# Kernel tuning notes

Hardware: AMD Instinct MI355X
Metric: run time of the kernel (lower is better)

## Reference

```python
import jax, jax.numpy as jnp
import numpy as np

D_MODEL = 1024
H = 16
D_K = D_MODEL // H
B, S = 4, 2048
NEG = -1000000000.0


def setup_inputs() -> dict:
    key = jax.random.key(0)
    ks = jax.random.split(key, 12)
    scale = 1.0 / np.sqrt(D_MODEL)
    inp = {
        "query": jax.random.normal(ks[0], (B, S, D_MODEL), jnp.float32),
        "key": jax.random.normal(ks[1], (B, S, D_MODEL), jnp.float32),
        "value": jax.random.normal(ks[2], (B, S, D_MODEL), jnp.float32),
        # causal lower-triangular mask, shape (B, S, S); forward unsqueezes head dim
        "mask": jnp.broadcast_to(jnp.tril(jnp.ones((S, S), jnp.int32)), (B, S, S)),
        "Wq": jax.random.normal(ks[3], (D_MODEL, D_MODEL), jnp.float32) * scale,
        "bq": jnp.zeros((D_MODEL,), jnp.float32),
        "Wk": jax.random.normal(ks[4], (D_MODEL, D_MODEL), jnp.float32) * scale,
        "bk": jnp.zeros((D_MODEL,), jnp.float32),
        "Wv": jax.random.normal(ks[5], (D_MODEL, D_MODEL), jnp.float32) * scale,
        "bv": jnp.zeros((D_MODEL,), jnp.float32),
        "Wo": jax.random.normal(ks[6], (D_MODEL, D_MODEL), jnp.float32) * scale,
        "bo": jnp.zeros((D_MODEL,), jnp.float32),
    }
    return inp


def reference(query, key, value, mask, Wq, bq, Wk, bk, Wv, bv, Wo, bo):
    b, s, _ = query.shape
    # projections (torch Linear: x @ W.T + b); split into heads -> (b, h, s, d_k)
    def proj(x, W, bias):
        return (x @ W.T + bias).reshape(b, -1, H, D_K).transpose(0, 2, 1, 3)

    Q = proj(query, Wq, bq)
    K = proj(key, Wk, bk)
    V = proj(value, Wv, bv)

    scores = jnp.einsum("bhqd,bhkd->bhqk", Q, K) / np.sqrt(D_K)
    m = mask[:, None, :, :]  # (b, 1, s, s)
    scores = jnp.where(m == 0, NEG, scores)
    attn = jax.nn.softmax(scores, axis=-1)
    x = jnp.einsum("bhqk,bhkd->bhqd", attn, V)
    x = x.transpose(0, 2, 1, 3).reshape(b, -1, D_MODEL)
    return x @ Wo.T + bo
```

## Files before the change

### kernel.cpp

```cpp
#include <hip/hip_runtime.h>
#include <hip/hip_bf16.h>

#define DMODEL 1024
#define NH 16
#define DKH 64
#define NB 4
#define SEQ 2048
#define MTOT (NB*SEQ)

typedef __bf16 bf16_t;
typedef __bf16 bf16x8 __attribute__((ext_vector_type(8)));
typedef float f32x4 __attribute__((ext_vector_type(4)));

__device__ __forceinline__ void async_copy16(void* lds, const void* g) {
    __builtin_amdgcn_global_load_lds(
        (const __attribute__((address_space(1))) unsigned int*)g,
        (__attribute__((address_space(3))) unsigned int*)lds, 16, 0, 0);
}

__device__ __forceinline__ float fast_exp2(float x) {
    return __builtin_amdgcn_exp2f(x);
}

__device__ __forceinline__ float rsum16(float v) {
    v += __shfl_xor(v, 1);
    v += __shfl_xor(v, 2);
    v += __shfl_xor(v, 4);
    v += __shfl_xor(v, 8);
    return v;
}

__global__ void cvt_kernel(const float* __restrict__ s0, const float* __restrict__ s1,
                           const float* __restrict__ s2, const float* __restrict__ s3,
                           bf16_t* __restrict__ d0, bf16_t* __restrict__ d1,
                           bf16_t* __restrict__ d2, bf16_t* __restrict__ d3, int n)
{
    const float* s = (blockIdx.y == 0) ? s0 : (blockIdx.y == 1) ? s1 :
                     (blockIdx.y == 2) ? s2 : s3;
    bf16_t* d = (blockIdx.y == 0) ? d0 : (blockIdx.y == 1) ? d1 :
                (blockIdx.y == 2) ? d2 : d3;
    int i = (blockIdx.x * 256 + threadIdx.x) * 8;
    if (i < n) {
        float4 a = *(const float4*)&s[i];
        float4 b = *(const float4*)&s[i + 4];
        union { bf16_t h[8]; uint4 u; } t;
        t.h[0]=(bf16_t)a.x; t.h[1]=(bf16_t)a.y; t.h[2]=(bf16_t)a.z; t.h[3]=(bf16_t)a.w;
        t.h[4]=(bf16_t)b.x; t.h[5]=(bf16_t)b.y; t.h[6]=(bf16_t)b.z; t.h[7]=(bf16_t)b.w;
        *(uint4*)&d[i] = t.u;
    }
}

template<int OUT_MODE>
__global__ __launch_bounds__(256, 2)
void gemm_bt(const bf16_t* __restrict__ A, const bf16_t* __restrict__ W,
             const float* __restrict__ bias, void* __restrict__ out,
             int M, int N, int K, float scale)
{
    __shared__ bf16_t As[2][128 * 64];
    __shared__ bf16_t Ws[2][128 * 64];

    const int tid  = threadIdx.x;
    const int wave = tid >> 6;
    const int lane = tid & 63;
    const int ln   = lane & 15;
    const int quad = lane >> 4;
    const int wm   = (wave >> 1) * 64;
    const int wn   = (wave & 1) * 64;
    const int bm   = blockIdx.x * 128;
    const int bn   = blockIdx.y * 128;
    const int srow = wave * 8 + (lane >> 3);
    const int sg   = (lane & 7) * 8;

    f32x4 acc[4][4] = {};

    #pragma unroll
    for (int rr = 0; rr < 4; ++rr) {
        int row = rr * 32 + srow;
        async_copy16(&As[0][(size_t)(rr * 32 + wave * 8) * 64],
                     &A[(size_t)(bm + row) * K + sg]);
        async_copy16(&Ws[0][(size_t)(rr * 32 + wave * 8) * 64],
                     &W[(size_t)(bn + row) * K + sg]);
    }

    int cur = 0;
    for (int k0 = 0; k0 < K; k0 += 64, cur ^= 1) {
        __syncthreads();

        if (k0 + 64 < K) {
            #pragma unroll
            for (int rr = 0; rr < 4; ++rr) {
                int row = rr * 32 + srow;
                async_copy16(&As[cur ^ 1][(size_t)(rr * 32 + wave * 8) * 64],
                             &A[(size_t)(bm + row) * K + k0 + 64 + sg]);
                async_copy16(&Ws[cur ^ 1][(size_t)(rr * 32 + wave * 8) * 64],
                             &W[(size_t)(bn + row) * K + k0 + 64 + sg]);
            }
        }

        bf16x8 af[2][4], wf[2][4];
        #pragma unroll
        for (int h = 0; h < 2; ++h)
            #pragma unroll
            for (int u = 0; u < 4; ++u) {
                af[h][u] = *(const bf16x8*)&As[cur][(wm + u * 16 + ln) * 64 + h * 32 + quad * 8];
                wf[h][u] = *(const bf16x8*)&Ws[cur][(wn + u * 16 + ln) * 64 + h * 32 + quad * 8];
            }
        #pragma unroll
        for (int h = 0; h < 2; ++h)
            #pragma unroll
            for (int im = 0; im < 4; ++im)
                #pragma unroll
                for (int jn = 0; jn < 4; ++jn)
                    acc[im][jn] = __builtin_amdgcn_mfma_f32_16x16x32_bf16(
                        af[h][im], wf[h][jn], acc[im][jn], 0, 0, 0);
    }

    #pragma unroll
    for (int jn = 0; jn < 4; ++jn) {
        int n = bn + wn + jn * 16 + ln;
        float bv = bias[n];
        #pragma unroll
        for (int im = 0; im < 4; ++im) {
            #pragma unroll
            for (int r = 0; r < 4; ++r) {
                int m = bm + wm + im * 16 + quad * 4 + r;
                float v = (acc[im][jn][r] + bv) * scale;
                if (OUT_MODE == 0) {
                    int b = m >> 11, s = m & (SEQ - 1);
                    int h = n >> 6, d = n & 63;
                    ((bf16_t*)out)[(((size_t)(b * NH + h)) * SEQ + s) * DKH + d] = (bf16_t)v;
                } else if (OUT_MODE == 2) {
                    int b = m >> 11, s = m & (SEQ - 1);
                    int h = n >> 6, d = n & 63;
                    ((bf16_t*)out)[(((size_t)(b * NH + h)) * DKH + d) * SEQ + s] = (bf16_t)v;
                } else {
                    ((float*)out)[(size_t)m * N + n] = v;
                }
            }
        }
    }
}

__global__ __launch_bounds__(256, 3)
void attn_kernel(const bf16_t* __restrict__ Q, const bf16_t* __restrict__ Km,
                 const bf16_t* __restrict__ Vt, bf16_t* __restrict__ X)
{
    __shared__ __align__(16) bf16_t Ks[2][64 * 64];
    __shared__ __align__(16) bf16_t Vs[2][64 * 64];
    __shared__ __align__(16) bf16_t Ps[4][32][72];

    const int tid  = threadIdx.x;
    const int wave = tid >> 6;
    const int lane = tid & 63;
    const int ln   = lane & 15;
    const int quad = lane >> 4;
    const int cs   = ln & 7;

    const int qt = (blockIdx.x + blockIdx.y + ((blockIdx.y >> 4) << 2)) & 15;
    const int bh = blockIdx.y;
    const int q0 = qt * 128;
    const size_t base = (size_t)bh * SEQ * DKH;

    bf16x8 aq[2][2];
    #pragma unroll
    for (int so = 0; so < 2; ++so) {
        const bf16_t* qr = Q + base + (size_t)(q0 + so * 64 + wave * 16 + ln) * DKH;
        aq[so][0] = *(const bf16x8*)(qr + quad * 8);
        aq[so][1] = *(const bf16x8*)(qr + 32 + quad * 8);
    }

    f32x4 oacc[2][4] = {};
    float psum[2][4] = {};

    const int nkt = 2 * qt + 2;

    const int srow8 = lane >> 3;
    const int schk  = lane & 7;

    #pragma unroll
    for (int qq = 0; qq < 2; ++qq) {
        const int rb  = wave * 16 + qq * 8;
        const int row = rb + srow8;
        const int csr = schk ^ (row & 7);
        async_copy16(&Ks[0][rb * 64], Km + base + (size_t)row * DKH + csr * 8);
        async_copy16(&Vs[0][rb * 64], Vt + base + (size_t)row * SEQ + csr * 8);
    }
    __syncthreads();

    int cur = 0;
    for (int kt = 0; kt < nkt; ++kt, cur ^= 1) {
        const int j0 = kt * 64;
        const bool skip0 = (kt == nkt - 1);

        if (kt + 1 < nkt) {
            const int jn0 = j0 + 64;
            #pragma unroll
            for (int qq = 0; qq < 2; ++qq) {
                const int rb  = wave * 16 + qq * 8;
                const int row = rb + srow8;
                const int csr = schk ^ (row & 7);
                async_copy16(&Ks[cur ^ 1][rb * 64],
                             Km + base + (size_t)(jn0 + row) * DKH + csr * 8);
                async_copy16(&Vs[cur ^ 1][rb * 64],
                             Vt + base + (size_t)row * SEQ + jn0 + csr * 8);
            }
        }

        bf16x8 kf[4][2];
        #pragma unroll
        for (int jn = 0; jn < 4; ++jn) {
            const int rr = (jn * 16 + ln) * 64;
            kf[jn][0] = *(const bf16x8*)&Ks[cur][rr + ((quad    ) ^ cs) * 8];
            kf[jn][1] = *(const bf16x8*)&Ks[cur][rr + ((4 + quad) ^ cs) * 8];
        }

        f32x4 s[2][4] = {};
        #pragma unroll
        for (int so = 0; so < 2; ++so) {
            if (so == 0 && skip0) continue;
            #pragma unroll
            for (int jn = 0; jn < 4; ++jn) {
                s[so][jn] = __builtin_amdgcn_mfma_f32_16x16x32_bf16(aq[so][0], kf[jn][0], s[so][jn], 0, 0, 0);
                s[so][jn] = __builtin_amdgcn_mfma_f32_16x16x32_bf16(aq[so][1], kf[jn][1], s[so][jn], 0, 0, 0);
            }
        }

        bf16x8 vf[4][2];
        #pragma unroll
        for (int nj = 0; nj < 4; ++nj) {
            const int rr = (nj * 16 + ln) * 64;
            vf[nj][0] = *(const bf16x8*)&Vs[cur][rr + ((quad    ) ^ cs) * 8];
            vf[nj][1] = *(const bf16x8*)&Vs[cur][rr + ((4 + quad) ^ cs) * 8];
        }

        #pragma unroll
        for (int so = 0; so < 2; ++so) {
            if (so == 0 && skip0) continue;
            const int rbase = q0 + so * 64 + wave * 16 + quad * 4;
            const bool diag = (j0 + 63 > q0 + so * 64);
            #pragma unroll
            for (int r = 0; r < 4; ++r) {
                float rowsum = 0.f;
                #pragma unroll
                for (int jn = 0; jn < 4; ++jn) {
                    float v = s[so][jn][r];
                    if (diag) {
                        int col = j0 + jn * 16 + ln;
                        if (col > rbase + r) v = -1e30f;
                    }
                    float p = fast_exp2(v);
                    s[so][jn][r] = p;
                    rowsum += p;
                }
                psum[so][r] += rowsum;
            }
            #pragma unroll
            for (int r = 0; r < 4; ++r)
                #pragma unroll
                for (int jn = 0; jn < 4; ++jn)
                    Ps[wave][so * 16 + quad * 4 + r][jn * 16 + ln] = (bf16_t)s[so][jn][r];
        }

        #pragma unroll
        for (int so = 0; so < 2; ++so) {
            if (so == 0 && skip0) continue;
            bf16x8 ap0 = *(const bf16x8*)&Ps[wave][so * 16 + ln][quad * 8];
            bf16x8 ap1 = *(const bf16x8*)&Ps[wave][so * 16 + ln][32 + quad * 8];
            #pragma unroll
            for (int nj = 0; nj < 4; ++nj) {
                oacc[so][nj] = __builtin_amdgcn_mfma_f32_16x16x32_bf16(ap0, vf[nj][0], oacc[so][nj], 0, 0, 0);
                oacc[so][nj] = __builtin_amdgcn_mfma_f32_16x16x32_bf16(ap1, vf[nj][1], oacc[so][nj], 0, 0, 0);
            }
        }

        __syncthreads();
    }

    const int bb = bh >> 4, hh = bh & 15;
    #pragma unroll
    for (int so = 0; so < 2; ++so) {
        #pragma unroll
        for (int r = 0; r < 4; ++r) {
            int sg = q0 + so * 64 + wave * 16 + quad * 4 + r;
            float inv = 1.f / rsum16(psum[so][r]);
            #pragma unroll
            for (int nj = 0; nj < 4; ++nj)
                X[((size_t)(bb * SEQ + sg)) * DMODEL + hh * DKH + nj * 16 + ln] =
                    (bf16_t)(oacc[so][nj][r] * inv);
        }
    }
}

extern "C" void kernel_launch(void* const* d_in, const int* in_sizes, int n_in,
                              void* d_out, int out_size, void* d_ws, size_t ws_size,
                              hipStream_t stream)
{
    const float* query = (const float*)d_in[0];
    const float* key   = (const float*)d_in[1];
    const float* value = (const float*)d_in[2];
    const float* Wq = (const float*)d_in[4];
    const float* bq = (const float*)d_in[5];
    const float* Wk = (const float*)d_in[6];
    const float* bk = (const float*)d_in[7];
    const float* Wv = (const float*)d_in[8];
    const float* bv = (const float*)d_in[9];
    const float* Wo = (const float*)d_in[10];
    const float* bo = (const float*)d_in[11];
    float* out = (float*)d_out;

    char* ws = (char*)d_ws;
    bf16_t* qb  = (bf16_t*)(ws);
    bf16_t* kb  = (bf16_t*)(ws + ((size_t)16 << 20));
    bf16_t* vb  = (bf16_t*)(ws + ((size_t)32 << 20));
    bf16_t* Qh  = (bf16_t*)(ws + ((size_t)48 << 20));
    bf16_t* Wqb = (bf16_t*)(ws + ((size_t)64 << 20));
    bf16_t* Wkb = (bf16_t*)(ws + ((size_t)66 << 20));
    bf16_t* Wvb = (bf16_t*)(ws + ((size_t)68 << 20));
    bf16_t* Wob = (bf16_t*)(ws + ((size_t)70 << 20));
    bf16_t* Kh  = qb;
    bf16_t* Vth = kb;
    bf16_t* X   = vb;

    const int nAct = MTOT * DMODEL;
    const int nW   = DMODEL * DMODEL;
    cvt_kernel<<<dim3(nAct / 2048, 3), 256, 0, stream>>>(query, key, value, query,
                                                         qb, kb, vb, qb, nAct);
    cvt_kernel<<<dim3(nW / 2048, 4), 256, 0, stream>>>(Wq, Wk, Wv, Wo,
                                                       Wqb, Wkb, Wvb, Wob, nW);

    dim3 gg(MTOT / 128, DMODEL / 128);
    dim3 bt(256);
    const float qscale = 0.125f * 1.4426950408889634f;
    gemm_bt<0><<<gg, bt, 0, stream>>>(qb, Wqb, bq, Qh,  MTOT, DMODEL, DMODEL, qscale);
    gemm_bt<0><<<gg, bt, 0, stream>>>(kb, Wkb, bk, Kh,  MTOT, DMODEL, DMODEL, 1.0f);
    gemm_bt<2><<<gg, bt, 0, stream>>>(vb, Wvb, bv, Vth, MTOT, DMODEL, DMODEL, 1.0f);

    attn_kernel<<<dim3(SEQ / 128, NB * NH), bt, 0, stream>>>(Qh, Kh, Vth, X);

    gemm_bt<1><<<gg, bt, 0, stream>>>(X, Wob, bo, out, MTOT, DMODEL, DMODEL, 1.0f);
}
```

Before: 398.3 us.

## Fuse QKV projections into one GEMM launch and single-buffer LDS tiles

Replaces three separate Q/K/V projection GEMM launches with one kernel whose grid covers all three output ranges, selecting the input, bias and output layout per block. GEMM kernels drop LDS double buffering for a single buffer with two barriers per k-step, raising the occupancy target to 3 blocks per CU. Intermediate K and V head buffers are relocated into the output buffer so inputs are not overwritten. This trades prefetch overlap for higher occupancy and fewer launches.

New measurement: 393.6 us. No clear change (-1.2%).

```diff
diff --git a/kernel.cpp b/kernel.cpp
--- a/kernel.cpp
+++ b/kernel.cpp
@@ -51,13 +51,13 @@
 }
 
 template<int OUT_MODE>
-__global__ __launch_bounds__(256, 2)
+__global__ __launch_bounds__(256, 3)
 void gemm_bt(const bf16_t* __restrict__ A, const bf16_t* __restrict__ W,
              const float* __restrict__ bias, void* __restrict__ out,
              int M, int N, int K, float scale)
 {
-    __shared__ bf16_t As[2][128 * 64];
-    __shared__ bf16_t Ws[2][128 * 64];
+    __shared__ bf16_t As[128 * 64];
+    __shared__ bf16_t Ws[128 * 64];
 
     const int tid  = threadIdx.x;
     const int wave = tid >> 6;
@@ -73,37 +73,24 @@
 
     f32x4 acc[4][4] = {};
 
-    #pragma unroll
-    for (int rr = 0; rr < 4; ++rr) {
-        int row = rr * 32 + srow;
-        async_copy16(&As[0][(size_t)(rr * 32 + wave * 8) * 64],
-                     &A[(size_t)(bm + row) * K + sg]);
-        async_copy16(&Ws[0][(size_t)(rr * 32 + wave * 8) * 64],
-                     &W[(size_t)(bn + row) * K + sg]);
-    }
-
-    int cur = 0;
-    for (int k0 = 0; k0 < K; k0 += 64, cur ^= 1) {
+    for (int k0 = 0; k0 < K; k0 += 64) {
+        #pragma unroll
+        for (int rr = 0; rr < 4; ++rr) {
+            int row = rr * 32 + srow;
+            async_copy16(&As[(size_t)(rr * 32 + wave * 8) * 64],
+                         &A[(size_t)(bm + row) * K + k0 + sg]);
+            async_copy16(&Ws[(size_t)(rr * 32 + wave * 8) * 64],
+                         &W[(size_t)(bn + row) * K + k0 + sg]);
+        }
         __syncthreads();
 
-        if (k0 + 64 < K) {
-            #pragma unroll
-            for (int rr = 0; rr < 4; ++rr) {
-                int row = rr * 32 + srow;
-                async_copy16(&As[cur ^ 1][(size_t)(rr * 32 + wave * 8) * 64],
-                             &A[(size_t)(bm + row) * K + k0 + 64 + sg]);
-                async_copy16(&Ws[cur ^ 1][(size_t)(rr * 32 + wave * 8) * 64],
-                             &W[(size_t)(bn + row) * K + k0 + 64 + sg]);
-            }
-        }
-
         bf16x8 af[2][4], wf[2][4];
         #pragma unroll
         for (int h = 0; h < 2; ++h)
             #pragma unroll
             for (int u = 0; u < 4; ++u) {
-                af[h][u] = *(const bf16x8*)&As[cur][(wm + u * 16 + ln) * 64 + h * 32 + quad * 8];
-                wf[h][u] = *(const bf16x8*)&Ws[cur][(wn + u * 16 + ln) * 64 + h * 32 + quad * 8];
+                af[h][u] = *(const bf16x8*)&As[(wm + u * 16 + ln) * 64 + h * 32 + quad * 8];
+                wf[h][u] = *(const bf16x8*)&Ws[(wn + u * 16 + ln) * 64 + h * 32 + quad * 8];
             }
         #pragma unroll
         for (int h = 0; h < 2; ++h)
@@ -113,6 +100,8 @@
                 for (int jn = 0; jn < 4; ++jn)
                     acc[im][jn] = __builtin_amdgcn_mfma_f32_16x16x32_bf16(
                         af[h][im], wf[h][jn], acc[im][jn], 0, 0, 0);
+
+        __syncthreads();
     }
 
     #pragma unroll
@@ -135,6 +124,92 @@
                     ((bf16_t*)out)[(((size_t)(b * NH + h)) * DKH + d) * SEQ + s] = (bf16_t)v;
                 } else {
                     ((float*)out)[(size_t)m * N + n] = v;
+                }
+            }
+        }
+    }
+}
+
+__global__ __launch_bounds__(256, 3)
+void gemm_qkv(const bf16_t* __restrict__ Aq, const bf16_t* __restrict__ Ak,
+              const bf16_t* __restrict__ Av, const bf16_t* __restrict__ W3,
+              const float* __restrict__ bqp, const float* __restrict__ bkp,
+              const float* __restrict__ bvp,
+              bf16_t* __restrict__ Qh, bf16_t* __restrict__ Kh,
+              bf16_t* __restrict__ Vth, float qscale)
+{
+    __shared__ bf16_t As[128 * 64];
+    __shared__ bf16_t Ws[128 * 64];
+
+    const int K    = DMODEL;
+    const int tid  = threadIdx.x;
+    const int wave = tid >> 6;
+    const int lane = tid & 63;
+    const int ln   = lane & 15;
+    const int quad = lane >> 4;
+    const int wm   = (wave >> 1) * 64;
+    const int wn   = (wave & 1) * 64;
+    const int bm   = blockIdx.x * 128;
+    const int bnG  = blockIdx.y * 128;
+    const int sel  = blockIdx.y >> 3;
+    const bf16_t* A = (sel == 0) ? Aq : (sel == 1) ? Ak : Av;
+    const int srow = wave * 8 + (lane >> 3);
+    const int sg   = (lane & 7) * 8;
+
+    f32x4 acc[4][4] = {};
+
+    for (int k0 = 0; k0 < K; k0 += 64) {
+        #pragma unroll
+        for (int rr = 0; rr < 4; ++rr) {
+            int row = rr * 32 + srow;
+            async_copy16(&As[(size_t)(rr * 32 + wave * 8) * 64],
+                         &A[(size_t)(bm + row) * K + k0 + sg]);
+            async_copy16(&Ws[(size_t)(rr * 32 + wave * 8) * 64],
+                         &W3[(size_t)(bnG + row) * K + k0 + sg]);
+        }
+        __syncthreads();
+
+        bf16x8 af[2][4], wf[2][4];
+        #pragma unroll
+        for (int h = 0; h < 2; ++h)
+            #pragma unroll
+            for (int u = 0; u < 4; ++u) {
+                af[h][u] = *(const bf16x8*)&As[(wm + u * 16 + ln) * 64 + h * 32 + quad * 8];
+                wf[h][u] = *(const bf16x8*)&Ws[(wn + u * 16 + ln) * 64 + h * 32 + quad * 8];
+            }
+        #pragma unroll
+        for (int h = 0; h < 2; ++h)
+            #pragma unroll
+            for (int im = 0; im < 4; ++im)
+                #pragma unroll
+                for (int jn = 0; jn < 4; ++jn)
+                    acc[im][jn] = __builtin_amdgcn_mfma_f32_16x16x32_bf16(
+                        af[h][im], wf[h][jn], acc[im][jn], 0, 0, 0);
+
+        __syncthreads();
+    }
+
+    const float* bias = (sel == 0) ? bqp : (sel == 1) ? bkp : bvp;
+    const float scale = (sel == 0) ? qscale : 1.0f;
+    const int bn = bnG & (DMODEL - 1);
+
+    #pragma unroll
+    for (int jn = 0; jn < 4; ++jn) {
+        int n = bn + wn + jn * 16 + ln;
+        float bv = bias[n];
+        int h = n >> 6, d = n & 63;
+        #pragma unroll
+        for (int im = 0; im < 4; ++im) {
+            #pragma unroll
+            for (int r = 0; r < 4; ++r) {
+                int m = bm + wm + im * 16 + quad * 4 + r;
+                float v = (acc[im][jn][r] + bv) * scale;
+                int b = m >> 11, s = m & (SEQ - 1);
+                if (sel == 2) {
+                    Vth[(((size_t)(b * NH + h)) * DKH + d) * SEQ + s] = (bf16_t)v;
+                } else {
+                    bf16_t* outp = (sel == 1) ? Kh : Qh;
+                    outp[(((size_t)(b * NH + h)) * SEQ + s) * DKH + d] = (bf16_t)v;
                 }
             }
         }
@@ -317,9 +392,9 @@
     bf16_t* Wkb = (bf16_t*)(ws + ((size_t)66 << 20));
     bf16_t* Wvb = (bf16_t*)(ws + ((size_t)68 << 20));
     bf16_t* Wob = (bf16_t*)(ws + ((size_t)70 << 20));
-    bf16_t* Kh  = qb;
-    bf16_t* Vth = kb;
-    bf16_t* X   = vb;
+    bf16_t* Kh  = (bf16_t*)d_out;
+    bf16_t* Vth = (bf16_t*)((char*)d_out + ((size_t)16 << 20));
+    bf16_t* X   = qb;
 
     const int nAct = MTOT * DMODEL;
     const int nW   = DMODEL * DMODEL;
@@ -328,14 +403,14 @@
     cvt_kernel<<<dim3(nW / 2048, 4), 256, 0, stream>>>(Wq, Wk, Wv, Wo,
                                                        Wqb, Wkb, Wvb, Wob, nW);
 
-    dim3 gg(MTOT / 128, DMODEL / 128);
     dim3 bt(256);
     const float qscale = 0.125f * 1.4426950408889634f;
-    gemm_bt<0><<<gg, bt, 0, stream>>>(qb, Wqb, bq, Qh,  MTOT, DMODEL, DMODEL, qscale);
-    gemm_bt<0><<<gg, bt, 0, stream>>>(kb, Wkb, bk, Kh,  MTOT, DMODEL, DMODEL, 1.0f);
-    gemm_bt<2><<<gg, bt, 0, stream>>>(vb, Wvb, bv, Vth, MTOT, DMODEL, DMODEL, 1.0f);
+
+    gemm_qkv<<<dim3(MTOT / 128, 3 * DMODEL / 128), bt, 0, stream>>>(
+        qb, kb, vb, Wqb, bq, bk, bv, Qh, Kh, Vth, qscale);
 
     attn_kernel<<<dim3(SEQ / 128, NB * NH), bt, 0, stream>>>(Qh, Kh, Vth, X);
 
-    gemm_bt<1><<<gg, bt, 0, stream>>>(X, Wob, bo, out, MTOT, DMODEL, DMODEL, 1.0f);
-}
+    gemm_bt<1><<<dim3(MTOT / 128, DMODEL / 128), bt, 0, stream>>>(
+        X, Wob, bo, out, MTOT, DMODEL, DMODEL, 1.0f);
+}
```
